# Optimization experiments

Measured on AMD Instinct MI355X. Metric: run time of the kernel, lower is better.

Reference implementation:

```python
import jax, jax.numpy as jnp
import numpy as np

N = 50000      # nodes
E = 1600000    # edges (avg degree 32)
IN, HID, OUT = 32, 32, 10
K = 2          # kernel_size (dim=1, degree=1 open B-spline -> basis (1-u, u))


def setup_inputs() -> dict:
    key = jax.random.key(0)
    ks = jax.random.split(key, 10)
    x = jax.random.normal(ks[0], (N, IN), dtype=jnp.float32)
    edge_index = jax.random.randint(ks[1], (2, E), 0, N, dtype=jnp.int64)
    edge_attr = jax.random.uniform(ks[2], (E, 1), dtype=jnp.float32)  # pseudo-coords in [0,1)
    s1 = 1.0 / np.sqrt(IN * K)
    s2 = 1.0 / np.sqrt(HID * K)
    W1 = jax.random.uniform(ks[3], (K, IN, HID), minval=-s1, maxval=s1, dtype=jnp.float32)
    root1 = jax.random.uniform(ks[4], (IN, HID), minval=-s1, maxval=s1, dtype=jnp.float32)
    b1 = jnp.zeros((HID,), jnp.float32)
    W2 = jax.random.uniform(ks[5], (K, HID, OUT), minval=-s2, maxval=s2, dtype=jnp.float32)
    root2 = jax.random.uniform(ks[6], (HID, OUT), minval=-s2, maxval=s2, dtype=jnp.float32)
    b2 = jnp.zeros((OUT,), jnp.float32)
    return {"x": x, "edge_index": edge_index, "edge_attr": edge_attr,
            "W1": W1, "root1": root1, "b1": b1,
            "W2": W2, "root2": root2, "b2": b2}


def spline_conv(x, edge_index, edge_attr, W, W_root, b):
    # SplineConv, dim=1, kernel_size=2, degree=1, aggr='mean', root_weight, bias.
    # Basis for pseudo u in [0,1): B_0(u) = 1-u, B_1(u) = u.
    src, dst = edge_index[0], edge_index[1]
    u = edge_attr[:, 0]                      # [E]
    h0 = x @ W[0]                            # [N, out] node-level transform, then gather
    h1 = x @ W[1]
    msg = (1.0 - u)[:, None] * h0[src] + u[:, None] * h1[src]   # [E, out]
    n = x.shape[0]
    agg = jax.ops.segment_sum(msg, dst, num_segments=n)
    deg = jax.ops.segment_sum(jnp.ones((src.shape[0],), x.dtype), dst, num_segments=n)
    mean = agg / jnp.maximum(deg, 1.0)[:, None]
    return mean + x @ W_root + b


def reference(x, edge_index, edge_attr, W1, root1, b1, W2, root2, b2):
    # Dropout is identity in eval mode.
    h = jax.nn.relu(spline_conv(x, edge_index, edge_attr, W1, root1, b1))
    h = spline_conv(h, edge_index, edge_attr, W2, root2, b2)
    return jax.nn.log_softmax(h, axis=1)
```

## Files before the change

### kernel.cpp

```cpp
#include <hip/hip_runtime.h>
#include <math.h>

#define GSHIFT 6
#define GSIZE  64
#define NBSZ   1024
#define EPB    4096
#define CAP    3072

#define UDEC1 0.00390625f
#define UDEC2 0.001953125f

__device__ __forceinline__ unsigned bf16rn(float f) {
    unsigned u = __float_as_uint(f);
    return (u + 0x7FFFu + ((u >> 16) & 1u)) >> 16;
}
__device__ __forceinline__ float bfl(unsigned v) { return __uint_as_float(v << 16); }
__device__ __forceinline__ float bfh(unsigned v) { return __uint_as_float(v & 0xFFFF0000u); }

__global__ __launch_bounds__(256) void k_prep(const float* __restrict__ x,
                                              unsigned* __restrict__ x_pk,
                                              int* __restrict__ bcount,
                                              int n, int NB) {
    int t = blockIdx.x * 256 + threadIdx.x;
    if (t < NB) bcount[t] = 0;
    if (t >= n) return;
    const float4* xp = (const float4*)(x + (size_t)t * 32);
    #pragma unroll
    for (int k = 0; k < 4; k++) {
        float4 a = xp[2 * k], c = xp[2 * k + 1];
        uint4 pk;
        pk.x = bf16rn(a.x) | (bf16rn(a.y) << 16);
        pk.y = bf16rn(a.z) | (bf16rn(a.w) << 16);
        pk.z = bf16rn(c.x) | (bf16rn(c.y) << 16);
        pk.w = bf16rn(c.z) | (bf16rn(c.w) << 16);
        *(uint4*)(x_pk + (size_t)t * 16 + k * 4) = pk;
    }
}

__global__ __launch_bounds__(1024) void k_part(const int* __restrict__ src,
                                               const int* __restrict__ dst,
                                               const float* __restrict__ attr,
                                               int* __restrict__ bcount,
                                               unsigned* __restrict__ su,
                                               int E_, int NB) {
    __shared__ int lh[NBSZ];
    __shared__ int lst[NBSZ];
    __shared__ int lcur[NBSZ];
    __shared__ int gbase[NBSZ];
    __shared__ int wsum[16];
    __shared__ __align__(16) unsigned srt[EPB];
    __shared__ unsigned short lbk[EPB];
    int tid = threadIdx.x, lane = tid & 63, w = tid >> 6;
    lh[tid] = 0;
    __syncthreads();
    int base = blockIdx.x * EPB;
    int d[4];
    unsigned rec[4];
    #pragma unroll
    for (int k = 0; k < 4; k++) {
        int e = base + k * 1024 + tid;
        bool val = e < E_;
        int dd = val ? dst[e] : 0;
        int s  = val ? src[e] : 0;
        float a = val ? attr[e] : 0.f;
        d[k] = val ? (dd >> GSHIFT) : -1;
        unsigned uq = (unsigned)(a * 256.0f);
        rec[k] = (unsigned)(s & 0xFFFF) | ((unsigned)(dd & (GSIZE - 1)) << 16) | (uq << 24);
        if (d[k] >= 0) atomicAdd(&lh[d[k]], 1);
    }
    __syncthreads();
    int v = lh[tid];
    int incl = v;
    #pragma unroll
    for (int o = 1; o < 64; o <<= 1) {
        int t2 = __shfl_up(incl, o);
        if (lane >= o) incl += t2;
    }
    if (lane == 63) wsum[w] = incl;
    __syncthreads();
    int woff = 0;
    for (int k = 0; k < w; k++) woff += wsum[k];
    int excl = woff + incl - v;
    lst[tid] = excl;
    lcur[tid] = excl;
    if (tid < NB) gbase[tid] = atomicAdd(&bcount[tid], v);
    __syncthreads();
    #pragma unroll
    for (int k = 0; k < 4; k++) {
        if (d[k] >= 0) {
            int pos = atomicAdd(&lcur[d[k]], 1);
            srt[pos] = rec[k];
            lbk[pos] = (unsigned short)d[k];
        }
    }
    __syncthreads();
    int total = E_ - base; if (total > EPB) total = EPB;
    for (int p = tid; p < total; p += 1024) {
        int b = lbk[p];
        su[(size_t)b * CAP + gbase[b] + (p - lst[b])] = srt[p];
    }
}

__global__ __launch_bounds__(512) void k_fused(const int* __restrict__ bcount,
                                               const unsigned* __restrict__ su,
                                               unsigned* __restrict__ su2,
                                               int* __restrict__ rowptr,
                                               int* __restrict__ deg,
                                               const unsigned* __restrict__ x_pk,
                                               const float* __restrict__ x,
                                               const float* __restrict__ W1,
                                               const float* __restrict__ root1,
                                               const float* __restrict__ b1,
                                               const float* __restrict__ W2,
                                               const float* __restrict__ root2,
                                               unsigned* __restrict__ gg,
                                               float* __restrict__ hr, int n) {
    __shared__ __align__(16) unsigned sorted[CAP];
    __shared__ __align__(16) unsigned accum[GSIZE * 32];
    __shared__ __align__(16) unsigned hlp[GSIZE * 16];
    __shared__ __align__(16) unsigned sw01[1024];
    __shared__ __align__(16) float sRt[1024];
    __shared__ unsigned sAD[320];
    __shared__ float sR2[320];
    __shared__ float sB1[32];
    __shared__ int hist[GSIZE], cur[GSIZE], sstart[GSIZE], sdeg[GSIZE];
    __shared__ int stot;

    int b = blockIdx.x, tid = threadIdx.x;
    size_t basee = (size_t)b * CAP;
    int cnt = bcount[b];
    int node0 = b << GSHIFT;

    if (tid < GSIZE) hist[tid] = 0;
    for (int i = tid; i < 1024; i += 512) {
        float w0 = W1[i];
        sw01[i] = bf16rn(w0) | (bf16rn(W1[1024 + i] - w0) << 16);
        sRt[i] = root1[i];
    }
    if (tid < 320) {
        float a0 = W2[tid];
        sAD[tid] = bf16rn(a0) | (bf16rn(W2[320 + tid] - a0) << 16);
        sR2[tid] = root2[tid];
    }
    if (tid < 32) sB1[tid] = b1[tid];
    __syncthreads();

    for (int e = tid * 4; e < cnt; e += 2048) {
        uint4 r4 = *(const uint4*)(su + basee + e);
        unsigned rr[4] = {r4.x, r4.y, r4.z, r4.w};
        #pragma unroll
        for (int k = 0; k < 4; k++)
            if (e + k < cnt) atomicAdd(&hist[(rr[k] >> 16) & 63], 1);
    }
    __syncthreads();

    if (tid < 64) {
        int v = hist[tid];
        int pv = (v + 3) & ~3;
        int incl = pv;
        #pragma unroll
        for (int o = 1; o < 64; o <<= 1) {
            int t2 = __shfl_up(incl, o);
            if (tid >= o) incl += t2;
        }
        int excl = incl - pv;
        cur[tid] = excl; sstart[tid] = excl; sdeg[tid] = v;
        int node = node0 + tid;
        if (node < n) { rowptr[node] = (int)basee + excl; deg[node] = v; }
        if (tid == 63) stot = excl + pv;
        for (int p = excl + v; p < excl + pv; p++) sorted[p] = 0;
    }
    __syncthreads();

    for (int e = tid * 4; e < cnt; e += 2048) {
        uint4 r4 = *(const uint4*)(su + basee + e);
        unsigned rr[4] = {r4.x, r4.y, r4.z, r4.w};
        #pragma unroll
        for (int k = 0; k < 4; k++) {
            if (e + k < cnt) {
                unsigned r = rr[k];
                int pos = atomicAdd(&cur[(r >> 16) & 63], 1);
                sorted[pos] = r;
            }
        }
    }
    __syncthreads();

    {
        int tot4 = stot >> 2;
        uint4* dp = (uint4*)(su2 + basee);
        for (int p = tid; p < tot4; p += 512)
            dp[p] = *(const uint4*)(sorted + p * 4);
    }
    {
        int nl = tid >> 3, q = tid & 3, half = (tid >> 2) & 1;
        int st = sstart[nl], dgi = sdeg[nl];
        int endl = st + dgi;
        int q4 = (dgi + 3) >> 2;
        int hq = q4 >> 1, rem = q4 & 1;
        int myq = hq + (half < rem ? 1 : 0);
        int e0 = st + (half * hq + min(half, rem)) * 4;
        float a0[8] = {0,0,0,0,0,0,0,0}, a1[8] = {0,0,0,0,0,0,0,0};
        for (int i = 0; i < myq; i++) {
            int e = e0 + i * 4;
            uint4 rq = *(const uint4*)(sorted + e);
            unsigned rr[4] = {rq.x, rq.y, rq.z, rq.w};
            #pragma unroll
            for (int k = 0; k < 4; k++) {
                bool v = (e + k) < endl;
                unsigned r = rr[k];
                uint4 g = *(const uint4*)(x_pk + (size_t)(r & 0xFFFFu) * 16 + q * 4);
                float wv = v ? 1.f : 0.f;
                float u = v ? fmaf((float)(r >> 24), UDEC1, UDEC2) : 0.f;
                unsigned gw[4] = {g.x, g.y, g.z, g.w};
                #pragma unroll
                for (int m2 = 0; m2 < 4; m2++) {
                    float fl = bfl(gw[m2]), fh = bfh(gw[m2]);
                    a0[2*m2]   = fmaf(wv, fl, a0[2*m2]);
                    a0[2*m2+1] = fmaf(wv, fh, a0[2*m2+1]);
                    a1[2*m2]   = fmaf(u, fl, a1[2*m2]);
                    a1[2*m2+1] = fmaf(u, fh, a1[2*m2+1]);
                }
            }
        }
        #pragma unroll
        for (int k = 0; k < 8; k++) {
            a0[k] += __shfl_xor(a0[k], 4);
            a1[k] += __shfl_xor(a1[k], 4);
        }
        if (half == 0) {
            #pragma unroll
            for (int k = 0; k < 8; k++)
                accum[nl * 32 + q * 8 + k] = bf16rn(a0[k]) | (bf16rn(a1[k]) << 16);
        }
    }
    __syncthreads();

    {
        int nl = tid >> 3, j = tid & 7;
        int node = node0 + nl;
        float invd = 1.0f / fmaxf((float)sdeg[nl], 1.0f);
        float4 hv = make_float4(sB1[4*j], sB1[4*j+1], sB1[4*j+2], sB1[4*j+3]);
        const float* xrow = x + (size_t)(node < n ? node : 0) * 32;
        for (int i = 0; i < 32; i++) {
            unsigned sp = accum[nl * 32 + i];
            float s0 = bfl(sp) * invd;
            float s1 = bfh(sp) * invd;
            float xi = xrow[i];
            uint4 wp = *(const uint4*)(sw01 + i * 32 + 4 * j);
            float4 rt = *(const float4*)(sRt + i * 32 + 4 * j);
            hv.x = fmaf(s0, bfl(wp.x), fmaf(s1, bfh(wp.x), fmaf(xi, rt.x, hv.x)));
            hv.y = fmaf(s0, bfl(wp.y), fmaf(s1, bfh(wp.y), fmaf(xi, rt.y, hv.y)));
            hv.z = fmaf(s0, bfl(wp.z), fmaf(s1, bfh(wp.z), fmaf(xi, rt.z, hv.z)));
            hv.w = fmaf(s0, bfl(wp.w), fmaf(s1, bfh(wp.w), fmaf(xi, rt.w, hv.w)));
        }
        hv.x = fmaxf(hv.x, 0.f); hv.y = fmaxf(hv.y, 0.f);
        hv.z = fmaxf(hv.z, 0.f); hv.w = fmaxf(hv.w, 0.f);
        hlp[nl * 16 + 2 * j]     = bf16rn(hv.x) | (bf16rn(hv.y) << 16);
        hlp[nl * 16 + 2 * j + 1] = bf16rn(hv.z) | (bf16rn(hv.w) << 16);
    }
    __syncthreads();

    {
        int nl = tid >> 3, j = tid & 7;
        int node = node0 + nl;
        if (node < n) {
            #pragma unroll
            for (int ci = 0; ci < 2; ci++) {
                int c = j + ci * 8;
                if (c < 10) {
                    float g0 = 0.f, gd = 0.f, gr = 0.f;
                    for (int i2 = 0; i2 < 16; i2++) {
                        unsigned hp = hlp[nl * 16 + i2];
                        float h0 = bfl(hp), h1 = bfh(hp);
                        int i = 2 * i2;
                        unsigned wa = sAD[i * 10 + c];
                        unsigned wb = sAD[(i + 1) * 10 + c];
                        g0 = fmaf(h0, bfl(wa), fmaf(h1, bfl(wb), g0));
                        gd = fmaf(h0, bfh(wa), fmaf(h1, bfh(wb), gd));
                        gr = fmaf(h0, sR2[i * 10 + c], fmaf(h1, sR2[(i + 1) * 10 + c], gr));
                    }
                    gg[(size_t)node * 16 + c] = bf16rn(g0) | (bf16rn(gd) << 16);
                    hr[(size_t)node * 10 + c] = gr;
                } else {
                    gg[(size_t)node * 16 + c] = 0;
                }
            }
        }
    }
}

__global__ __launch_bounds__(256) void k_agg2(const int* __restrict__ rowptr,
                                              const int* __restrict__ deg,
                                              const unsigned* __restrict__ su2,
                                              const unsigned* __restrict__ gg,
                                              const float* __restrict__ hr,
                                              const float* __restrict__ b2,
                                              float* __restrict__ out, int n) {
    int lane = threadIdx.x & 63;
    int node = (blockIdx.x * 4 + (threadIdx.x >> 6)) * 4 + (lane >> 4);
    int qt = (lane >> 2) & 3;
    int q  = lane & 3;
    if (node >= n) return;
    int start = rowptr[node], dgi = deg[node], end = start + dgi;
    int q4 = (dgi + 3) >> 2;
    int qb = q4 >> 2, rem = q4 & 3;
    int myq = qb + (qt < rem ? 1 : 0);
    int e0 = start + (qt * qb + min(qt, rem)) * 4;
    float acc[4] = {0, 0, 0, 0};
    for (int i = 0; i < myq; i++) {
        int e = e0 + i * 4;
        uint4 rq = *(const uint4*)(su2 + e);
        unsigned rr[4] = {rq.x, rq.y, rq.z, rq.w};
        #pragma unroll
        for (int k = 0; k < 4; k++) {
            bool v = (e + k) < end;
            unsigned r = rr[k];
            uint4 g = *(const uint4*)(gg + (size_t)(r & 0xFFFFu) * 16 + q * 4);
            float wv = v ? 1.f : 0.f;
            float u = v ? fmaf((float)(r >> 24), UDEC1, UDEC2) : 0.f;
            acc[0] = fmaf(wv, bfl(g.x), fmaf(u, bfh(g.x), acc[0]));
            acc[1] = fmaf(wv, bfl(g.y), fmaf(u, bfh(g.y), acc[1]));
            acc[2] = fmaf(wv, bfl(g.z), fmaf(u, bfh(g.z), acc[2]));
            acc[3] = fmaf(wv, bfl(g.w), fmaf(u, bfh(g.w), acc[3]));
        }
    }
    #pragma unroll
    for (int k = 0; k < 4; k++) {
        acc[k] += __shfl_xor(acc[k], 4);
        acc[k] += __shfl_xor(acc[k], 8);
    }
    float invd = 1.0f / fmaxf((float)dgi, 1.0f);
    int c0 = q * 4;
    float lg[4];
    float m = -INFINITY;
    #pragma unroll
    for (int k = 0; k < 4; k++) {
        int c = c0 + k;
        if (c < 10) {
            lg[k] = fmaf(acc[k], invd, hr[(size_t)node * 10 + c] + b2[c]);
            m = fmaxf(m, lg[k]);
        } else lg[k] = -INFINITY;
    }
    m = fmaxf(m, __shfl_xor(m, 1));
    m = fmaxf(m, __shfl_xor(m, 2));
    float ex = 0.f;
    #pragma unroll
    for (int k = 0; k < 4; k++)
        if (c0 + k < 10) ex += __expf(lg[k] - m);
    ex += __shfl_xor(ex, 1);
    ex += __shfl_xor(ex, 2);
    float lse = m + __logf(ex);
    if (qt == 0 && c0 < 10) {
        *(float2*)(out + (size_t)node * 10 + c0) =
            make_float2(lg[0] - lse, lg[1] - lse);
        if (c0 + 2 < 10)
            *(float2*)(out + (size_t)node * 10 + c0 + 2) =
                make_float2(lg[2] - lse, lg[3] - lse);
    }
}

extern "C" void kernel_launch(void* const* d_in, const int* in_sizes, int n_in,
                              void* d_out, int out_size, void* d_ws, size_t ws_size,
                              hipStream_t stream) {
    const float* x     = (const float*)d_in[0];
    const int*   ei    = (const int*)d_in[1];
    const float* attr  = (const float*)d_in[2];
    const float* W1    = (const float*)d_in[3];
    const float* root1 = (const float*)d_in[4];
    const float* b1    = (const float*)d_in[5];
    const float* W2    = (const float*)d_in[6];
    const float* root2 = (const float*)d_in[7];
    const float* b2    = (const float*)d_in[8];
    float* out = (float*)d_out;

    int N_ = in_sizes[0] / 32;
    int E_ = in_sizes[1] / 2;
    const int* src = ei;
    const int* dst = ei + E_;
    int NB = (N_ + GSIZE - 1) >> GSHIFT;
    int NP = (E_ + EPB - 1) / EPB;

    char* ws = (char*)d_ws;
    size_t off = 0;
    auto alloc = [&](size_t bytes) -> void* {
        void* p = ws + off;
        off += (bytes + 255) & ~(size_t)255;
        return p;
    };
    int*      bcount = (int*)     alloc((size_t)NB * 4);
    unsigned* su     = (unsigned*)alloc(((size_t)NB * CAP + 64) * 4);
    unsigned* su2    = (unsigned*)alloc(((size_t)NB * CAP + 64) * 4);
    int*      rowptr = (int*)     alloc((size_t)N_ * 4);
    int*      deg    = (int*)     alloc((size_t)N_ * 4);
    unsigned* x_pk   = (unsigned*)alloc((size_t)N_ * 16 * 4);
    unsigned* gg     = (unsigned*)alloc((size_t)N_ * 16 * 4);
    float*    hr     = (float*)   alloc((size_t)N_ * 10 * 4);

    int prep_blocks = (N_ > NB ? N_ : NB);
    k_prep <<<(prep_blocks + 255) / 256, 256, 0, stream>>>(x, x_pk, bcount, N_, NB);
    k_part <<<NP, 1024, 0, stream>>>(src, dst, attr, bcount, su, E_, NB);
    k_fused<<<NB, 512, 0, stream>>>(bcount, su, su2, rowptr, deg, x_pk, x,
                                    W1, root1, b1, W2, root2, gg, hr, N_);
    k_agg2 <<<(N_ + 15) / 16, 256, 0, stream>>>(rowptr, deg, su2, gg, hr, b2, out, N_);
}
```

Baseline: 75.64 us.

## Partition edges into coarser 256-node buckets and filter per 64-node quarter in fused kernel

Result: slower. 80.01 us (+5.8%).

```diff
diff --git a/kernel.cpp b/kernel.cpp
--- a/kernel.cpp
+++ b/kernel.cpp
@@ -1,11 +1,13 @@
 #include <hip/hip_runtime.h>
 #include <math.h>
 
+#define CSHIFT 8
+#define CSIZE  256
 #define GSHIFT 6
 #define GSIZE  64
-#define NBSZ   1024
 #define EPB    4096
-#define CAP    3072
+#define CAPC   9728
+#define CAP2   3072
 
 #define UDEC1 0.00390625f
 #define UDEC2 0.001953125f
@@ -20,9 +22,9 @@
 __global__ __launch_bounds__(256) void k_prep(const float* __restrict__ x,
                                               unsigned* __restrict__ x_pk,
                                               int* __restrict__ bcount,
-                                              int n, int NB) {
+                                              int n, int NBC) {
     int t = blockIdx.x * 256 + threadIdx.x;
-    if (t < NB) bcount[t] = 0;
+    if (t < NBC) bcount[t] = 0;
     if (t >= n) return;
     const float4* xp = (const float4*)(x + (size_t)t * 32);
     #pragma unroll
@@ -42,16 +44,16 @@
                                                const float* __restrict__ attr,
                                                int* __restrict__ bcount,
                                                unsigned* __restrict__ su,
-                                               int E_, int NB) {
-    __shared__ int lh[NBSZ];
-    __shared__ int lst[NBSZ];
-    __shared__ int lcur[NBSZ];
-    __shared__ int gbase[NBSZ];
-    __shared__ int wsum[16];
+                                               int E_, int NBC) {
+    __shared__ int lh[CSIZE];
+    __shared__ int lst[CSIZE];
+    __shared__ int lcur[CSIZE];
+    __shared__ int gbase[CSIZE];
+    __shared__ int wsum[4];
     __shared__ __align__(16) unsigned srt[EPB];
-    __shared__ unsigned short lbk[EPB];
+    __shared__ unsigned char lbk[EPB];
     int tid = threadIdx.x, lane = tid & 63, w = tid >> 6;
-    lh[tid] = 0;
+    if (tid < CSIZE) lh[tid] = 0;
     __syncthreads();
     int base = blockIdx.x * EPB;
     int d[4];
@@ -63,41 +65,46 @@
         int dd = val ? dst[e] : 0;
         int s  = val ? src[e] : 0;
         float a = val ? attr[e] : 0.f;
-        d[k] = val ? (dd >> GSHIFT) : -1;
+        d[k] = val ? (dd >> CSHIFT) : -1;
         unsigned uq = (unsigned)(a * 256.0f);
-        rec[k] = (unsigned)(s & 0xFFFF) | ((unsigned)(dd & (GSIZE - 1)) << 16) | (uq << 24);
+        rec[k] = (unsigned)(s & 0xFFFF) | ((unsigned)(dd & 255) << 16) | (uq << 24);
         if (d[k] >= 0) atomicAdd(&lh[d[k]], 1);
     }
     __syncthreads();
-    int v = lh[tid];
-    int incl = v;
-    #pragma unroll
-    for (int o = 1; o < 64; o <<= 1) {
-        int t2 = __shfl_up(incl, o);
-        if (lane >= o) incl += t2;
-    }
-    if (lane == 63) wsum[w] = incl;
-    __syncthreads();
-    int woff = 0;
-    for (int k = 0; k < w; k++) woff += wsum[k];
-    int excl = woff + incl - v;
-    lst[tid] = excl;
-    lcur[tid] = excl;
-    if (tid < NB) gbase[tid] = atomicAdd(&bcount[tid], v);
+    int v = 0, incl = 0;
+    if (tid < CSIZE) {
+        v = lh[tid];
+        incl = v;
+        #pragma unroll
+        for (int o = 1; o < 64; o <<= 1) {
+            int t2 = __shfl_up(incl, o);
+            if (lane >= o) incl += t2;
+        }
+        if (lane == 63) wsum[w] = incl;
+    }
+    __syncthreads();
+    if (tid < CSIZE) {
+        int woff = 0;
+        for (int k = 0; k < w; k++) woff += wsum[k];
+        int excl = woff + incl - v;
+        lst[tid] = excl;
+        lcur[tid] = excl;
+        if (tid < NBC) gbase[tid] = atomicAdd(&bcount[tid], v);
+    }
     __syncthreads();
     #pragma unroll
     for (int k = 0; k < 4; k++) {
         if (d[k] >= 0) {
             int pos = atomicAdd(&lcur[d[k]], 1);
             srt[pos] = rec[k];
-            lbk[pos] = (unsigned short)d[k];
+            lbk[pos] = (unsigned char)d[k];
         }
     }
     __syncthreads();
     int total = E_ - base; if (total > EPB) total = EPB;
     for (int p = tid; p < total; p += 1024) {
         int b = lbk[p];
-        su[(size_t)b * CAP + gbase[b] + (p - lst[b])] = srt[p];
+        su[(size_t)b * CAPC + gbase[b] + (p - lst[b])] = srt[p];
     }
 }
 
@@ -115,7 +122,7 @@
                                                const float* __restrict__ root2,
                                                unsigned* __restrict__ gg,
                                                float* __restrict__ hr, int n) {
-    __shared__ __align__(16) unsigned sorted[CAP];
+    __shared__ __align__(16) unsigned sorted[CAP2];
     __shared__ __align__(16) unsigned accum[GSIZE * 32];
     __shared__ __align__(16) unsigned hlp[GSIZE * 16];
     __shared__ __align__(16) unsigned sw01[1024];
@@ -127,8 +134,10 @@
     __shared__ int stot;
 
     int b = blockIdx.x, tid = threadIdx.x;
-    size_t basee = (size_t)b * CAP;
-    int cnt = bcount[b];
+    int cb = b >> 2, qd = b & 3;
+    size_t basee = (size_t)cb * CAPC;
+    size_t basee2 = (size_t)b * CAP2;
+    int cnt = bcount[cb];
     int node0 = b << GSHIFT;
 
     if (tid < GSIZE) hist[tid] = 0;
@@ -149,8 +158,12 @@
         uint4 r4 = *(const uint4*)(su + basee + e);
         unsigned rr[4] = {r4.x, r4.y, r4.z, r4.w};
         #pragma unroll
-        for (int k = 0; k < 4; k++)
-            if (e + k < cnt) atomicAdd(&hist[(rr[k] >> 16) & 63], 1);
+        for (int k = 0; k < 4; k++) {
+            if (e + k < cnt) {
+                unsigned loc8 = (rr[k] >> 16) & 255u;
+                if ((int)(loc8 >> 6) == qd) atomicAdd(&hist[loc8 & 63], 1);
+            }
+        }
     }
     __syncthreads();
 
@@ -166,7 +179,7 @@
         int excl = incl - pv;
         cur[tid] = excl; sstart[tid] = excl; sdeg[tid] = v;
         int node = node0 + tid;
-        if (node < n) { rowptr[node] = (int)basee + excl; deg[node] = v; }
+        if (node < n) { rowptr[node] = (int)basee2 + excl; deg[node] = v; }
         if (tid == 63) stot = excl + pv;
         for (int p = excl + v; p < excl + pv; p++) sorted[p] = 0;
     }
@@ -179,8 +192,11 @@
         for (int k = 0; k < 4; k++) {
             if (e + k < cnt) {
                 unsigned r = rr[k];
-                int pos = atomicAdd(&cur[(r >> 16) & 63], 1);
-                sorted[pos] = r;
+                unsigned loc8 = (r >> 16) & 255u;
+                if ((int)(loc8 >> 6) == qd) {
+                    int pos = atomicAdd(&cur[loc8 & 63], 1);
+                    sorted[pos] = r;
+                }
             }
         }
     }
@@ -188,7 +204,7 @@
 
     {
         int tot4 = stot >> 2;
-        uint4* dp = (uint4*)(su2 + basee);
+        uint4* dp = (uint4*)(su2 + basee2);
         for (int p = tid; p < tot4; p += 512)
             dp[p] = *(const uint4*)(sorted + p * 4);
     }
@@ -378,8 +394,9 @@
     int E_ = in_sizes[1] / 2;
     const int* src = ei;
     const int* dst = ei + E_;
-    int NB = (N_ + GSIZE - 1) >> GSHIFT;
-    int NP = (E_ + EPB - 1) / EPB;
+    int NBC = (N_ + CSIZE - 1) >> CSHIFT;
+    int NBF = (N_ + GSIZE - 1) >> GSHIFT;
+    int NP  = (E_ + EPB - 1) / EPB;
 
     char* ws = (char*)d_ws;
     size_t off = 0;
@@ -388,19 +405,18 @@
         off += (bytes + 255) & ~(size_t)255;
         return p;
     };
-    int*      bcount = (int*)     alloc((size_t)NB * 4);
-    unsigned* su     = (unsigned*)alloc(((size_t)NB * CAP + 64) * 4);
-    unsigned* su2    = (unsigned*)alloc(((size_t)NB * CAP + 64) * 4);
+    int*      bcount = (int*)     alloc((size_t)NBC * 4);
+    unsigned* su     = (unsigned*)alloc(((size_t)NBC * CAPC + 64) * 4);
+    unsigned* su2    = (unsigned*)alloc(((size_t)NBF * CAP2 + 64) * 4);
     int*      rowptr = (int*)     alloc((size_t)N_ * 4);
     int*      deg    = (int*)     alloc((size_t)N_ * 4);
     unsigned* x_pk   = (unsigned*)alloc((size_t)N_ * 16 * 4);
     unsigned* gg     = (unsigned*)alloc((size_t)N_ * 16 * 4);
     float*    hr     = (float*)   alloc((size_t)N_ * 10 * 4);
 
-    int prep_blocks = (N_ > NB ? N_ : NB);
-    k_prep <<<(prep_blocks + 255) / 256, 256, 0, stream>>>(x, x_pk, bcount, N_, NB);
-    k_part <<<NP, 1024, 0, stream>>>(src, dst, attr, bcount, su, E_, NB);
-    k_fused<<<NB, 512, 0, stream>>>(bcount, su, su2, rowptr, deg, x_pk, x,
-                                    W1, root1, b1, W2, root2, gg, hr, N_);
+    k_prep <<<(N_ + 255) / 256, 256, 0, stream>>>(x, x_pk, bcount, N_, NBC);
+    k_part <<<NP, 1024, 0, stream>>>(src, dst, attr, bcount, su, E_, NBC);
+    k_fused<<<NBF, 512, 0, stream>>>(bcount, su, su2, rowptr, deg, x_pk, x,
+                                     W1, root1, b1, W2, root2, gg, hr, N_);
     k_agg2 <<<(N_ + 15) / 16, 256, 0, stream>>>(rowptr, deg, su2, gg, hr, b2, out, N_);
 }
```
